# Performance work log

Hardware: AMD Instinct MI355X
Metric: run time of the kernel (lower is better)

The kernel has to match this reference:

```python
import jax, jax.numpy as jnp
import numpy as np

EPS = 1e-6

def setup_inputs() -> dict:
    key = jax.random.key(0)
    k1, k2, k3, k4, k5 = jax.random.split(key, 5)
    B, Lq, Lk, D, Dc = 8, 1024, 8192, 256, 128
    q = jax.random.normal(k1, (B, Lq, D), dtype=jnp.float32)
    k_q = jax.random.randint(k2, (B, Lk, Dc), 0, 16, dtype=jnp.int32)  # 4-bit codes
    k_scale = jax.random.uniform(k3, (B, 1, Dc), dtype=jnp.float32)
    k_zero = jax.random.uniform(k4, (B, 1, Dc), dtype=jnp.float32) * 15.0
    W_up = jax.random.normal(k5, (D, Dc), dtype=jnp.float32) / np.sqrt(Dc)
    return {"q": q, "k_q": k_q, "k_scale": k_scale, "k_zero": k_zero, "W_up": W_up}

def reference(q, k_q, k_scale, k_zero, W_up):
    # int4 dequantization: (B, Lk, Dc)
    k_c = k_scale * (k_q.astype(jnp.float32) - k_zero)
    # low-rank decompress (nn.Linear(d_compressed, d_model, bias=False)): k = k_c @ W_up.T -> (B, Lk, D)
    k = jnp.einsum('blc,dc->bld', k_c, W_up)
    # squared norms (raw values used in diff, clamped values used in denominator)
    q_sq = jnp.sum(q * q, axis=-1)  # (B, Lq)
    k_sq = jnp.sum(k * k, axis=-1)  # (B, Lk)
    q_norm_sq = jnp.minimum(q_sq, 1.0 - EPS)
    k_norm_sq = jnp.minimum(k_sq, 1.0 - EPS)
    # ||q_i - k_j||^2 via expansion (same math as materializing the diff tensor)
    qk = jnp.einsum('bqd,bkd->bqk', q, k)  # (B, Lq, Lk)
    diff_norm_sq = jnp.maximum(q_sq[:, :, None] + k_sq[:, None, :] - 2.0 * qk, 0.0)
    denom = (1.0 - q_norm_sq)[:, :, None] * (1.0 - k_norm_sq)[:, None, :] + EPS
    dist = jnp.arccosh(1.0 + 2.0 * diff_norm_sq / denom)  # (B, Lq, Lk)
    return dist
```

## Files before the change

kernel.cpp:

```cpp
#include <hip/hip_runtime.h>
#include <hip/hip_bf16.h>

#define B_   8
#define LQ   1024
#define LK   8192
#define D_   256
#define DC   128
#define EPSF 1e-6f

typedef __attribute__((ext_vector_type(8))) short short8;
typedef __attribute__((ext_vector_type(4))) float floatx4;

static __device__ __forceinline__ floatx4 mfma16(short8 a, short8 b, floatx4 c) {
    return __builtin_amdgcn_mfma_f32_16x16x32_bf16(a, b, c, 0, 0, 0);
}
static __device__ __forceinline__ float fast_rcp(float x)  { return __builtin_amdgcn_rcpf(x); }
static __device__ __forceinline__ float fast_sqrt(float x) { return __builtin_amdgcn_sqrtf(x); }
static __device__ __forceinline__ float fast_ln(float x)   { return 0.69314718056f * __builtin_amdgcn_logf(x); }

__global__ void k_G(const float* __restrict__ W, __hip_bfloat16* __restrict__ G) {
    int c1 = blockIdx.x, c2 = threadIdx.x;
    float a0 = 0.f, a1 = 0.f, a2 = 0.f, a3 = 0.f;
#pragma unroll 4
    for (int d = 0; d < D_; d += 4) {
        a0 += W[(d + 0) * DC + c1] * W[(d + 0) * DC + c2];
        a1 += W[(d + 1) * DC + c1] * W[(d + 1) * DC + c2];
        a2 += W[(d + 2) * DC + c1] * W[(d + 2) * DC + c2];
        a3 += W[(d + 3) * DC + c1] * W[(d + 3) * DC + c2];
    }
    G[c1 * DC + c2] = __float2bfloat16((a0 + a1) + (a2 + a3));
}

__global__ __launch_bounds__(256) void k_qsq(const float* __restrict__ q,
                                             float* __restrict__ q_sq) {
    int row  = blockIdx.x * 4 + (threadIdx.x >> 6);
    int lane = threadIdx.x & 63;
    float4 v = *(const float4*)(q + (size_t)row * D_ + lane * 4);
    float s = v.x * v.x + v.y * v.y + v.z * v.z + v.w * v.w;
    for (int m = 1; m < 64; m <<= 1) s += __shfl_xor(s, m);
    if (lane == 0) q_sq[row] = s;
}

__global__ __launch_bounds__(256) void k_qproj(const float* __restrict__ q,
                                               const float* __restrict__ W,
                                               __hip_bfloat16* __restrict__ qproj) {
    __shared__ __hip_bfloat16 sA[64 * 72];
    __shared__ __hip_bfloat16 sB[128 * 72];
    int t = threadIdx.x, lane = t & 63, w = t >> 6;
    int quad = lane >> 4, li = lane & 15;
    int row0 = blockIdx.x * 64;

    floatx4 acc[8];
#pragma unroll
    for (int nt = 0; nt < 8; ++nt) acc[nt] = (floatx4){0.f, 0.f, 0.f, 0.f};

    for (int kc4 = 0; kc4 < 4; ++kc4) {
#pragma unroll
        for (int it = 0; it < 4; ++it) {
            int idx = it * 256 + t;
            int r = idx >> 4, pos = idx & 15;
            float4 v = *(const float4*)(q + (size_t)(row0 + r) * D_ + kc4 * 64 + pos * 4);
            __hip_bfloat16* dst = &sA[r * 72 + pos * 4];
            dst[0] = __float2bfloat16(v.x); dst[1] = __float2bfloat16(v.y);
            dst[2] = __float2bfloat16(v.z); dst[3] = __float2bfloat16(v.w);
        }
#pragma unroll
        for (int it = 0; it < 32; ++it) {
            int e = it * 256 + t;
            int dl = e >> 7, c = e & 127;
            sB[c * 72 + dl] = __float2bfloat16(W[(size_t)(kc4 * 64 + dl) * DC + c]);
        }
        __syncthreads();
        short8 af[2];
#pragma unroll
        for (int ks = 0; ks < 2; ++ks)
            af[ks] = *(const short8*)&sA[(w * 16 + li) * 72 + ks * 32 + quad * 8];
#pragma unroll
        for (int nt = 0; nt < 8; ++nt)
#pragma unroll
            for (int ks = 0; ks < 2; ++ks) {
                short8 bf = *(const short8*)&sB[(nt * 16 + li) * 72 + ks * 32 + quad * 8];
                acc[nt] = mfma16(af[ks], bf, acc[nt]);
            }
        __syncthreads();
    }
#pragma unroll
    for (int nt = 0; nt < 8; ++nt)
#pragma unroll
        for (int r = 0; r < 4; ++r) {
            int row = w * 16 + quad * 4 + r;
            qproj[(size_t)(row0 + row) * DC + nt * 16 + li] = __float2bfloat16(acc[nt][r]);
        }
}

__global__ __launch_bounds__(256) void k_dq_ksq(const int* __restrict__ kq,
                                                const float* __restrict__ kscale,
                                                const float* __restrict__ kzero,
                                                const __hip_bfloat16* __restrict__ G,
                                                __hip_bfloat16* __restrict__ kc,
                                                float* __restrict__ k_sq) {
    __shared__ __hip_bfloat16 sK[128 * 132];
    int t = threadIdx.x, lane = t & 63, w = t >> 6;
    int quad = lane >> 4, li = lane & 15;
    int b = blockIdx.x >> 6, l0 = (blockIdx.x & 63) * 128;

    const int4* codes = (const int4*)(kq + ((size_t)b * LK + l0) * DC);
    int col = (t & 31) * 4;
    float4 sc = *(const float4*)(kscale + b * DC + col);
    float4 zp = *(const float4*)(kzero + b * DC + col);
    __hip_bfloat16* kco = kc + ((size_t)b * LK + l0) * DC;
#pragma unroll
    for (int it = 0; it < 16; ++it) {
        int idx = it * 256 + t;
        int r = idx >> 5;
        int4 c4 = codes[idx];
        __hip_bfloat16 tmp[4];
        tmp[0] = __float2bfloat16(sc.x * ((float)c4.x - zp.x));
        tmp[1] = __float2bfloat16(sc.y * ((float)c4.y - zp.y));
        tmp[2] = __float2bfloat16(sc.z * ((float)c4.z - zp.z));
        tmp[3] = __float2bfloat16(sc.w * ((float)c4.w - zp.w));
        *(uint2*)&sK[r * 132 + col] = *(const uint2*)tmp;
        *(uint2*)(kco + idx * 4)    = *(const uint2*)tmp;
    }
    __syncthreads();

    short8 af[2][4];
#pragma unroll
    for (int mt = 0; mt < 2; ++mt)
#pragma unroll
        for (int ks = 0; ks < 4; ++ks)
            af[mt][ks] = *(const short8*)&sK[(w * 32 + mt * 16 + li) * 132 + ks * 32 + quad * 8];
    float s[2][4] = {{0, 0, 0, 0}, {0, 0, 0, 0}};
#pragma unroll
    for (int nt = 0; nt < 8; ++nt) {
        floatx4 a0 = (floatx4){0.f, 0.f, 0.f, 0.f};
        floatx4 a1 = (floatx4){0.f, 0.f, 0.f, 0.f};
#pragma unroll
        for (int ks = 0; ks < 4; ++ks) {
            short8 bf = *(const short8*)(G + (size_t)(nt * 16 + li) * DC + ks * 32 + quad * 8);
            a0 = mfma16(af[0][ks], bf, a0);
            a1 = mfma16(af[1][ks], bf, a1);
        }
        int c2 = nt * 16 + li;
#pragma unroll
        for (int r = 0; r < 4; ++r) {
            int r0 = w * 32 +      quad * 4 + r;
            int r1 = w * 32 + 16 + quad * 4 + r;
            s[0][r] += a0[r] * __bfloat162float(sK[r0 * 132 + c2]);
            s[1][r] += a1[r] * __bfloat162float(sK[r1 * 132 + c2]);
        }
    }
#pragma unroll
    for (int mt = 0; mt < 2; ++mt)
#pragma unroll
        for (int r = 0; r < 4; ++r) {
            float v = s[mt][r];
            v += __shfl_xor(v, 1); v += __shfl_xor(v, 2);
            v += __shfl_xor(v, 4); v += __shfl_xor(v, 8);
            if (li == 0)
                k_sq[(size_t)b * LK + l0 + w * 32 + mt * 16 + quad * 4 + r] = v;
        }
}

__global__ __launch_bounds__(256) void k_main(const __hip_bfloat16* __restrict__ qproj,
                                              const __hip_bfloat16* __restrict__ kc,
                                              const float* __restrict__ q_sq,
                                              const float* __restrict__ k_sq,
                                              float* __restrict__ out) {
    __shared__ __hip_bfloat16 sA[128 * 72];
    __shared__ __hip_bfloat16 sB[128 * 72];
    int t = threadIdx.x, lane = t & 63, w = t >> 6;
    int quad = lane >> 4, li = lane & 15;
    int wm = w >> 1, wn = w & 1;
    int n0 = blockIdx.x * 128, m0 = blockIdx.y * 128, b = blockIdx.z;
    const uint4* Ag = (const uint4*)(qproj + ((size_t)b * LQ + m0) * DC);
    const uint4* Bg = (const uint4*)(kc   + ((size_t)b * LK + n0) * DC);
    uint4* dA = (uint4*)sA; uint4* dB = (uint4*)sB;

    floatx4 acc[4][4];
#pragma unroll
    for (int i = 0; i < 4; ++i)
#pragma unroll
        for (int j = 0; j < 4; ++j)
            acc[i][j] = (floatx4){0.f, 0.f, 0.f, 0.f};

    int r_ = t >> 3, ch_ = t & 7;
    uint4 ra[4], rb[4];
#pragma unroll
    for (int it = 0; it < 4; ++it) {
        ra[it] = Ag[(it * 32 + r_) * 16 + ch_];
        rb[it] = Bg[(it * 32 + r_) * 16 + ch_];
    }
#pragma unroll
    for (int it = 0; it < 4; ++it) {
        dA[(it * 32 + r_) * 9 + ch_] = ra[it];
        dB[(it * 32 + r_) * 9 + ch_] = rb[it];
    }
    __syncthreads();
#pragma unroll
    for (int it = 0; it < 4; ++it) {
        ra[it] = Ag[(it * 32 + r_) * 16 + 8 + ch_];
        rb[it] = Bg[(it * 32 + r_) * 16 + 8 + ch_];
    }
#pragma unroll
    for (int ks = 0; ks < 2; ++ks) {
        short8 af[4], bfr[4];
#pragma unroll
        for (int i = 0; i < 4; ++i) {
            af[i]  = *(const short8*)&sA[(wm * 64 + i * 16 + li) * 72 + ks * 32 + quad * 8];
            bfr[i] = *(const short8*)&sB[(wn * 64 + i * 16 + li) * 72 + ks * 32 + quad * 8];
        }
#pragma unroll
        for (int i = 0; i < 4; ++i)
#pragma unroll
            for (int j = 0; j < 4; ++j)
                acc[i][j] = mfma16(af[i], bfr[j], acc[i][j]);
    }
    __syncthreads();
#pragma unroll
    for (int it = 0; it < 4; ++it) {
        dA[(it * 32 + r_) * 9 + ch_] = ra[it];
        dB[(it * 32 + r_) * 9 + ch_] = rb[it];
    }
    __syncthreads();
#pragma unroll
    for (int ks = 0; ks < 2; ++ks) {
        short8 af[4], bfr[4];
#pragma unroll
        for (int i = 0; i < 4; ++i) {
            af[i]  = *(const short8*)&sA[(wm * 64 + i * 16 + li) * 72 + ks * 32 + quad * 8];
            bfr[i] = *(const short8*)&sB[(wn * 64 + i * 16 + li) * 72 + ks * 32 + quad * 8];
        }
#pragma unroll
        for (int i = 0; i < 4; ++i)
#pragma unroll
            for (int j = 0; j < 4; ++j)
                acc[i][j] = mfma16(af[i], bfr[j], acc[i][j]);
    }

    float ksv[4], knv[4];
#pragma unroll
    for (int j = 0; j < 4; ++j) {
        ksv[j] = k_sq[(size_t)b * LK + n0 + wn * 64 + j * 16 + li];
        knv[j] = 1.f - fminf(ksv[j], 1.f - EPSF);
    }
#pragma unroll
    for (int i = 0; i < 4; ++i) {
#pragma unroll
        for (int r = 0; r < 4; ++r) {
            int mrow = m0 + wm * 64 + i * 16 + quad * 4 + r;
            size_t gm = (size_t)b * LQ + mrow;
            float qs  = q_sq[gm];
            float omq = 1.f - fminf(qs, 1.f - EPSF);
            float* orow = out + gm * LK + n0 + wn * 64;
#pragma unroll
            for (int j = 0; j < 4; ++j) {
                float diff  = fmaxf(qs + ksv[j] - 2.f * acc[i][j][r], 0.f);
                float delta = 2.f * diff * fast_rcp(omq * knv[j] + EPSF);
                float sq    = fast_sqrt(delta * (delta + 2.f));
                orow[j * 16 + li] = fast_ln(1.f + delta + sq);
            }
        }
    }
}

extern "C" void kernel_launch(void* const* d_in, const int* in_sizes, int n_in,
                              void* d_out, int out_size, void* d_ws, size_t ws_size,
                              hipStream_t stream) {
    const float* q      = (const float*)d_in[0];
    const int*   kq     = (const int*)d_in[1];
    const float* kscale = (const float*)d_in[2];
    const float* kzero  = (const float*)d_in[3];
    const float* W      = (const float*)d_in[4];
    float* out = (float*)d_out;

    char* ws = (char*)d_ws;
    __hip_bfloat16* qproj = (__hip_bfloat16*)(ws);
    __hip_bfloat16* kc    = (__hip_bfloat16*)(ws + 2097152);
    __hip_bfloat16* G     = (__hip_bfloat16*)(ws + 18874368);
    float*          q_sq  = (float*)(ws + 18907136);
    float*          k_sq  = (float*)(ws + 18939904);

    k_G     <<<128, 128, 0, stream>>>(W, G);
    k_qsq   <<<2048, 256, 0, stream>>>(q, q_sq);
    k_qproj <<<128, 256, 0, stream>>>(q, W, qproj);
    k_dq_ksq<<<512, 256, 0, stream>>>(kq, kscale, kzero, G, kc, k_sq);
    dim3 grid(LK / 128, LQ / 128, B_);
    k_main  <<<grid, 256, 0, stream>>>(qproj, kc, q_sq, k_sq, out);
}
```

Measured before the change: 405.6 us.

## Transpose MFMA operands for vectorized nontemporal output stores; fuse q_sq into qproj

The main kernel swaps the MFMA operand order so each lane holds four consecutive key columns for one query row. It then computes the arccosh epilogue and writes the output with 128-bit nontemporal stores instead of scalar strided stores. The q squared-norm kernel is folded into the q projection kernel, and the Gram kernel splits its reduction across two thread halves. The aim is to make the large output write (256 MB) more bandwidth-efficient and to cut launch count, at the cost of slightly more complex indexing.

```diff
diff --git a/kernel.cpp b/kernel.cpp
--- a/kernel.cpp
+++ b/kernel.cpp
@@ -18,38 +18,37 @@
 static __device__ __forceinline__ float fast_sqrt(float x) { return __builtin_amdgcn_sqrtf(x); }
 static __device__ __forceinline__ float fast_ln(float x)   { return 0.69314718056f * __builtin_amdgcn_logf(x); }
 
-__global__ void k_G(const float* __restrict__ W, __hip_bfloat16* __restrict__ G) {
-    int c1 = blockIdx.x, c2 = threadIdx.x;
+__global__ __launch_bounds__(256) void k_G(const float* __restrict__ W,
+                                           __hip_bfloat16* __restrict__ G) {
+    __shared__ float red[128];
+    int c1 = blockIdx.x;
+    int t = threadIdx.x, c2 = t & 127, h = t >> 7;
+    int d0 = h * 128;
     float a0 = 0.f, a1 = 0.f, a2 = 0.f, a3 = 0.f;
 #pragma unroll 4
-    for (int d = 0; d < D_; d += 4) {
-        a0 += W[(d + 0) * DC + c1] * W[(d + 0) * DC + c2];
-        a1 += W[(d + 1) * DC + c1] * W[(d + 1) * DC + c2];
-        a2 += W[(d + 2) * DC + c1] * W[(d + 2) * DC + c2];
-        a3 += W[(d + 3) * DC + c1] * W[(d + 3) * DC + c2];
-    }
-    G[c1 * DC + c2] = __float2bfloat16((a0 + a1) + (a2 + a3));
-}
-
-__global__ __launch_bounds__(256) void k_qsq(const float* __restrict__ q,
-                                             float* __restrict__ q_sq) {
-    int row  = blockIdx.x * 4 + (threadIdx.x >> 6);
-    int lane = threadIdx.x & 63;
-    float4 v = *(const float4*)(q + (size_t)row * D_ + lane * 4);
-    float s = v.x * v.x + v.y * v.y + v.z * v.z + v.w * v.w;
-    for (int m = 1; m < 64; m <<= 1) s += __shfl_xor(s, m);
-    if (lane == 0) q_sq[row] = s;
+    for (int d = 0; d < 128; d += 4) {
+        a0 += W[(size_t)(d0 + d + 0) * DC + c1] * W[(size_t)(d0 + d + 0) * DC + c2];
+        a1 += W[(size_t)(d0 + d + 1) * DC + c1] * W[(size_t)(d0 + d + 1) * DC + c2];
+        a2 += W[(size_t)(d0 + d + 2) * DC + c1] * W[(size_t)(d0 + d + 2) * DC + c2];
+        a3 += W[(size_t)(d0 + d + 3) * DC + c1] * W[(size_t)(d0 + d + 3) * DC + c2];
+    }
+    float s = (a0 + a1) + (a2 + a3);
+    if (h) red[c2] = s;
+    __syncthreads();
+    if (!h) G[c1 * DC + c2] = __float2bfloat16(s + red[c2]);
 }
 
 __global__ __launch_bounds__(256) void k_qproj(const float* __restrict__ q,
                                                const float* __restrict__ W,
-                                               __hip_bfloat16* __restrict__ qproj) {
+                                               __hip_bfloat16* __restrict__ qproj,
+                                               float* __restrict__ q_sq) {
     __shared__ __hip_bfloat16 sA[64 * 72];
     __shared__ __hip_bfloat16 sB[128 * 72];
     int t = threadIdx.x, lane = t & 63, w = t >> 6;
     int quad = lane >> 4, li = lane & 15;
     int row0 = blockIdx.x * 64;
 
+    float psum[4] = {0.f, 0.f, 0.f, 0.f};
     floatx4 acc[8];
 #pragma unroll
     for (int nt = 0; nt < 8; ++nt) acc[nt] = (floatx4){0.f, 0.f, 0.f, 0.f};
@@ -60,6 +59,7 @@
             int idx = it * 256 + t;
             int r = idx >> 4, pos = idx & 15;
             float4 v = *(const float4*)(q + (size_t)(row0 + r) * D_ + kc4 * 64 + pos * 4);
+            psum[it] += v.x * v.x + v.y * v.y + v.z * v.z + v.w * v.w;
             __hip_bfloat16* dst = &sA[r * 72 + pos * 4];
             dst[0] = __float2bfloat16(v.x); dst[1] = __float2bfloat16(v.y);
             dst[2] = __float2bfloat16(v.z); dst[3] = __float2bfloat16(v.w);
@@ -91,6 +91,13 @@
             int row = w * 16 + quad * 4 + r;
             qproj[(size_t)(row0 + row) * DC + nt * 16 + li] = __float2bfloat16(acc[nt][r]);
         }
+#pragma unroll
+    for (int it = 0; it < 4; ++it) {
+        float s = psum[it];
+        s += __shfl_xor(s, 1); s += __shfl_xor(s, 2);
+        s += __shfl_xor(s, 4); s += __shfl_xor(s, 8);
+        if (li == 0) q_sq[row0 + it * 16 + w * 4 + quad] = s;
+    }
 }
 
 __global__ __launch_bounds__(256) void k_dq_ksq(const int* __restrict__ kq,
@@ -204,17 +211,17 @@
     }
 #pragma unroll
     for (int ks = 0; ks < 2; ++ks) {
-        short8 af[4], bfr[4];
+        short8 qf[4], kf[4];
 #pragma unroll
         for (int i = 0; i < 4; ++i) {
-            af[i]  = *(const short8*)&sA[(wm * 64 + i * 16 + li) * 72 + ks * 32 + quad * 8];
-            bfr[i] = *(const short8*)&sB[(wn * 64 + i * 16 + li) * 72 + ks * 32 + quad * 8];
+            qf[i] = *(const short8*)&sA[(wm * 64 + i * 16 + li) * 72 + ks * 32 + quad * 8];
+            kf[i] = *(const short8*)&sB[(wn * 64 + i * 16 + li) * 72 + ks * 32 + quad * 8];
         }
 #pragma unroll
         for (int i = 0; i < 4; ++i)
 #pragma unroll
             for (int j = 0; j < 4; ++j)
-                acc[i][j] = mfma16(af[i], bfr[j], acc[i][j]);
+                acc[i][j] = mfma16(kf[j], qf[i], acc[i][j]);
     }
     __syncthreads();
 #pragma unroll
@@ -225,41 +232,44 @@
     __syncthreads();
 #pragma unroll
     for (int ks = 0; ks < 2; ++ks) {
-        short8 af[4], bfr[4];
+        short8 qf[4], kf[4];
 #pragma unroll
         for (int i = 0; i < 4; ++i) {
-            af[i]  = *(const short8*)&sA[(wm * 64 + i * 16 + li) * 72 + ks * 32 + quad * 8];
-            bfr[i] = *(const short8*)&sB[(wn * 64 + i * 16 + li) * 72 + ks * 32 + quad * 8];
+            qf[i] = *(const short8*)&sA[(wm * 64 + i * 16 + li) * 72 + ks * 32 + quad * 8];
+            kf[i] = *(const short8*)&sB[(wn * 64 + i * 16 + li) * 72 + ks * 32 + quad * 8];
         }
 #pragma unroll
         for (int i = 0; i < 4; ++i)
 #pragma unroll
             for (int j = 0; j < 4; ++j)
-                acc[i][j] = mfma16(af[i], bfr[j], acc[i][j]);
-    }
-
-    float ksv[4], knv[4];
+                acc[i][j] = mfma16(kf[j], qf[i], acc[i][j]);
+    }
+
+    floatx4 ks4[4], kn4[4];
 #pragma unroll
     for (int j = 0; j < 4; ++j) {
-        ksv[j] = k_sq[(size_t)b * LK + n0 + wn * 64 + j * 16 + li];
-        knv[j] = 1.f - fminf(ksv[j], 1.f - EPSF);
+        ks4[j] = *(const floatx4*)(k_sq + (size_t)b * LK + n0 + wn * 64 + j * 16 + quad * 4);
+#pragma unroll
+        for (int r = 0; r < 4; ++r)
+            kn4[j][r] = 1.f - fminf(ks4[j][r], 1.f - EPSF);
     }
 #pragma unroll
     for (int i = 0; i < 4; ++i) {
-#pragma unroll
-        for (int r = 0; r < 4; ++r) {
-            int mrow = m0 + wm * 64 + i * 16 + quad * 4 + r;
-            size_t gm = (size_t)b * LQ + mrow;
-            float qs  = q_sq[gm];
-            float omq = 1.f - fminf(qs, 1.f - EPSF);
-            float* orow = out + gm * LK + n0 + wn * 64;
-#pragma unroll
-            for (int j = 0; j < 4; ++j) {
-                float diff  = fmaxf(qs + ksv[j] - 2.f * acc[i][j][r], 0.f);
-                float delta = 2.f * diff * fast_rcp(omq * knv[j] + EPSF);
+        int m = m0 + wm * 64 + i * 16 + li;
+        float qs  = q_sq[(size_t)b * LQ + m];
+        float omq = 1.f - fminf(qs, 1.f - EPSF);
+        float* orow = out + ((size_t)b * LQ + m) * (size_t)LK + n0 + wn * 64;
+#pragma unroll
+        for (int j = 0; j < 4; ++j) {
+            floatx4 o;
+#pragma unroll
+            for (int r = 0; r < 4; ++r) {
+                float diff  = fmaxf(qs + ks4[j][r] - 2.f * acc[i][j][r], 0.f);
+                float delta = 2.f * diff * fast_rcp(omq * kn4[j][r] + EPSF);
                 float sq    = fast_sqrt(delta * (delta + 2.f));
-                orow[j * 16 + li] = fast_ln(1.f + delta + sq);
+                o[r] = fast_ln(1.f + delta + sq);
             }
+            __builtin_nontemporal_store(o, (floatx4*)(orow + j * 16 + quad * 4));
         }
     }
 }
@@ -281,9 +291,8 @@
     float*          q_sq  = (float*)(ws + 18907136);
     float*          k_sq  = (float*)(ws + 18939904);
 
-    k_G     <<<128, 128, 0, stream>>>(W, G);
-    k_qsq   <<<2048, 256, 0, stream>>>(q, q_sq);
-    k_qproj <<<128, 256, 0, stream>>>(q, W, qproj);
+    k_G     <<<128, 256, 0, stream>>>(W, G);
+    k_qproj <<<128, 256, 0, stream>>>(q, W, qproj, q_sq);
     k_dq_ksq<<<512, 256, 0, stream>>>(kq, kscale, kzero, G, kc, k_sq);
     dim3 grid(LK / 128, LQ / 128, B_);
     k_main  <<<grid, 256, 0, stream>>>(qproj, kc, q_sq, k_sq, out);
```

Measured after the change: 384.4 us. -5.2%, faster.
